# Kernel tuning notes

Hardware: AMD Instinct MI355X
Metric: run time of the kernel (lower is better)

The kernel has to match this reference:

```python
import jax, jax.numpy as jnp
import numpy as np

NTA = 65536   # total atoms across all crystals
NC = 1024     # number of crystals
NO = 256      # descriptor output dim (desc.NO)
H = 332       # int(NO * 1.3) hidden dim of per-species MLP
S = 4         # number of species


def setup_inputs() -> dict:
    key = jax.random.key(0)
    ks = jax.random.split(key, 8)
    symbols = jax.random.randint(ks[0], (NTA,), 0, S)
    positions = jax.random.normal(ks[1], (NTA, 3), jnp.float32) * 3.0
    cells = jax.random.normal(ks[2], (NC, 3, 3), jnp.float32)
    pbcs = jnp.ones((NC, 3), dtype=bool)
    energyidx = jnp.arange(NC)
    crystalidx = jax.random.randint(ks[3], (NTA,), 0, NC)
    # stand-in descriptor projection (replaces external REANN desc module)
    Wd = jax.random.normal(ks[4], (3, NO), jnp.float32) * 0.5
    # stacked per-species MLP params: Linear(NO,H) -> SiLU -> Linear(H,1)
    W1 = jax.random.normal(ks[5], (S, NO, H), jnp.float32) / np.sqrt(NO).astype(np.float32)
    b1 = jnp.zeros((S, H), jnp.float32)
    W2 = jax.random.normal(ks[6], (S, H), jnp.float32) / np.sqrt(H).astype(np.float32)
    b2 = jnp.zeros((S,), jnp.float32)
    return {
        "symbols": symbols, "positions": positions, "cells": cells,
        "pbcs": pbcs, "energyidx": energyidx, "crystalidx": crystalidx,
        "Wd": Wd, "W1": W1, "b1": b1, "W2": W2, "b2": b2,
    }


def _atomic_energies(positions, symbols, Wd, W1, b1, W2, b2):
    # stand-in descriptor: [NTA, NO]
    feat = jnp.tanh(positions @ Wd)
    n_species = W1.shape[0]
    e = jnp.zeros((positions.shape[0],), feat.dtype)
    # species-routed small MLPs: dense compute + select (fixed small loop over species)
    for s in range(n_species):
        h = jax.nn.silu(feat @ W1[s] + b1[s])       # [NTA, H]
        es = h @ W2[s] + b2[s]                      # [NTA]
        e = jnp.where(symbols == s, es, e)
    return e


def reference(symbols, positions, cells, pbcs, energyidx, crystalidx, Wd, W1, b1, W2, b2):
    num_crystals = energyidx.shape[0]

    def total_energy(pos):
        en = _atomic_energies(pos, symbols, Wd, W1, b1, W2, b2)   # [NTA]
        E = jax.ops.segment_sum(en, crystalidx, num_segments=num_crystals)  # [NC]
        return jnp.sum(E), (en, E)

    # torch code: forces = grad(sum(energy), positions)  (positive gradient)
    forces, (energies, energy) = jax.grad(total_energy, has_aux=True)(positions)
    return (energies, energy, forces)
```

## Files before the change

kernel.cpp:

```cpp
#include <hip/hip_runtime.h>

#define NTA 65536
#define NC 1024
#define NO 256
#define HDIM 332
#define HP 352
#define NSP 4
#define NOUT (NTA + NC + NTA*3)
#define SORT_CAP (NTA + 4*128)

#define DP_STRIDE 720
#define LDS_MAIN  159744

typedef __attribute__((ext_vector_type(8))) short short8;
typedef __attribute__((ext_vector_type(4))) float f32x4;

#define OFF_CNT   0
#define OFF_CUR   64
#define OFF_START 128
#define OFF_FLAG  160
#define OFF_SORT  256
#define OFF_B1P   264448
#define OFF_W2P   270080
#define OFF_W1T   275712
#define OFF_W1P   996608
#define OFF_FACC  1717504

__device__ __forceinline__ unsigned short f2bf(float f){
  unsigned int u = __builtin_bit_cast(unsigned int, f);
  u += 0x7fffu + ((u>>16)&1u);
  return (unsigned short)(u>>16);
}
__device__ __forceinline__ float bf2f(unsigned short h){
  unsigned int u = ((unsigned int)h)<<16;
  return __builtin_bit_cast(float, u);
}
__device__ __forceinline__ float ldf(const void* p, int idx, int isbf){
  if (isbf) return bf2f(((const unsigned short*)p)[idx]);
  return ((const float*)p)[idx];
}
__device__ __forceinline__ float rcpf(float x){ return __builtin_amdgcn_rcpf(x); }

__global__ void k_init(float* __restrict__ acc, unsigned int* __restrict__ wshead,
                       int* __restrict__ sorted, const unsigned short* __restrict__ posu,
                       unsigned int* __restrict__ flag){
  int i = blockIdx.x*256 + threadIdx.x;
  acc[i] = 0.f;
  if (i < 32) wshead[i] = 0u;
  if (i < SORT_CAP) sorted[i] = -1;
  if (blockIdx.x == 1027 && threadIdx.x < 64){
    unsigned short u = posu[2*threadIdx.x];
    int e = (u>>7)&0xFF;
    bool inr = (e >= 110 && e <= 140);
    unsigned long long m = __ballot(inr);
    if (threadIdx.x == 0) flag[0] = (__popcll(m) >= 32) ? 1u : 0u;
  }
}

__global__ void k_count(const int* __restrict__ sym, unsigned int* __restrict__ cnt){
  __shared__ unsigned int h[NSP];
  int t = threadIdx.x;
  if (t < NSP) h[t] = 0u;
  __syncthreads();
  int i = blockIdx.x*256 + t;
  atomicAdd(&h[sym[i]], 1u);
  __syncthreads();
  if (t < NSP) atomicAdd(&cnt[t], h[t]);
}

__global__ void k_starts(const unsigned int* __restrict__ cnt, int* __restrict__ starts){
  if (threadIdx.x == 0){
    int a = 0; starts[0] = 0;
    for (int s=0;s<NSP;s++){ a += (int)(((cnt[s]+127u)>>7)<<7); starts[s+1] = a; }
  }
}

__global__ void k_scatter(const int* __restrict__ sym, const int* __restrict__ starts,
                          unsigned int* __restrict__ cur, int* __restrict__ sorted){
  int i = blockIdx.x*256 + threadIdx.x;
  int s = sym[i];
  int lane = threadIdx.x & 63;
  #pragma unroll
  for (int ss=0; ss<NSP; ss++){
    unsigned long long m = __ballot(s==ss);
    if (s == ss){
      int leader = __builtin_ctzll(m);
      int cw = __popcll(m);
      unsigned int b = 0;
      if (lane == leader) b = atomicAdd(&cur[ss], (unsigned int)cw);
      b = (unsigned int)__shfl((int)b, leader);
      int rank = __popcll(m & ((1ull<<lane) - 1ull));
      sorted[starts[ss] + (int)b + rank] = i;
    }
  }
}

__global__ void k_prepw(const void* __restrict__ W1, const void* __restrict__ b1,
                        const void* __restrict__ W2, const unsigned int* __restrict__ flag,
                        unsigned short* __restrict__ w1t, unsigned short* __restrict__ w1p,
                        float* __restrict__ b1p, float* __restrict__ w2p){
  const int isbf = (int)flag[0];
  int idx = blockIdx.x*256 + threadIdx.x;
  int s = idx / (HP*NO);
  int r = idx % (HP*NO);
  int j = r / NO;
  int i = r % NO;
  float v = (j < HDIM) ? ldf(W1, (s*NO + i)*HDIM + j, isbf) : 0.f;
  unsigned short hv = f2bf(v);
  w1t[(s*HP + j)*NO + i] = hv;
  w1p[(s*NO + i)*HP + j] = hv;
  if (i == 0){
    b1p[s*HP + j] = (j < HDIM) ? ldf(b1, s*HDIM + j, isbf) : 0.f;
    w2p[s*HP + j] = (j < HDIM) ? ldf(W2, s*HDIM + j, isbf) : 0.f;
  }
}

__global__ __launch_bounds__(512,2) void k_main(
    const int* __restrict__ sorted, const int* __restrict__ starts,
    const void* __restrict__ pos, const void* __restrict__ Wd,
    const unsigned short* __restrict__ W1T, const unsigned short* __restrict__ W1P,
    const float* __restrict__ b1p, const float* __restrict__ w2p,
    const void* __restrict__ b2g, const int* __restrict__ crys,
    const unsigned int* __restrict__ flag,
    float* __restrict__ Eatom, float* __restrict__ Ecry, float* __restrict__ forces)
{
  extern __shared__ char smem[];
  ushort4* wdT = (ushort4*)smem;
  char* featB  = smem + 2048;
  char* dpB    = smem + 2048 + 65536;
  float* Epart = (float*)dpB;
  float* Fpart = (float*)(dpB + 4096);

  const int base = blockIdx.x*128;
  if (base >= starts[4]) return;
  const int isbf = (int)flag[0];
  int sp = 0;
  #pragma unroll
  for (int s=1;s<NSP;s++) sp = (base >= starts[s]) ? s : sp;

  const int tid = threadIdx.x;
  const int l = tid & 63;
  const int w = tid >> 6;
  const int c = l & 15;
  const int g = l >> 4;

  if (tid < 256){
    float x = ldf(Wd, tid, isbf), y = ldf(Wd, NO+tid, isbf), z = ldf(Wd, 2*NO+tid, isbf);
    ushort4 u; u.x = f2bf(x); u.y = f2bf(y); u.z = f2bf(z); u.w = 0;
    wdT[tid] = u;
  }
  __syncthreads();

  {
    const int m = tid & 127;
    const int h = tid >> 7;
    int a = sorted[base + m];
    float px=0.f, py=0.f, pz=0.f;
    if (a >= 0){ px = ldf(pos,3*a,isbf); py = ldf(pos,3*a+1,isbf); pz = ldf(pos,3*a+2,isbf); }
    const int swz = (m&7)<<4;
    char* rowp = featB + m*512;
    #pragma unroll
    for (int k8=0;k8<8;k8++){
      int i0 = h*64 + k8*8;
      unsigned int pk[4];
      #pragma unroll
      for (int p2=0;p2<4;p2++){
        unsigned short hv[2];
        #pragma unroll
        for (int e2=0;e2<2;e2++){
          ushort4 wv = wdT[i0 + 2*p2 + e2];
          float v = px*bf2f(wv.x) + py*bf2f(wv.y) + pz*bf2f(wv.z);
          float e = __expf(2.f*v);
          hv[e2] = f2bf(1.f - 2.f*rcpf(e+1.f));
        }
        pk[p2] = (unsigned int)hv[0] | ((unsigned int)hv[1]<<16);
      }
      *(uint4*)(rowp + ((i0*2) ^ swz)) = make_uint4(pk[0],pk[1],pk[2],pk[3]);
    }
  }
  __syncthreads();

  const unsigned short* W1Ts = W1T + sp*HP*NO;
  const int fr0 = (w<6) ? w*3 : 18 + (w-6)*2;
  const int nT  = (w<6) ? 3 : 2;
  f32x4 acc[3][8];
  #pragma unroll
  for (int t=0;t<3;t++)
    #pragma unroll
    for (int nb=0;nb<8;nb++) acc[t][nb] = f32x4{0.f,0.f,0.f,0.f};

  #pragma unroll
  for (int kk=0; kk<8; kk++){
    short8 bfr[8];
    #pragma unroll
    for (int nb=0;nb<8;nb++){
      int m = nb*16 + c;
      bfr[nb] = *(const short8*)(featB + m*512 + ((kk*64 + g*16) ^ ((m&7)<<4)));
    }
    #pragma unroll
    for (int t=0;t<3;t++){
      if (t < nT){
        const short8 afr = *(const short8*)((const char*)W1Ts + ((fr0+t)*16 + c)*512 + kk*64 + g*16);
        #pragma unroll
        for (int nb=0;nb<8;nb++)
          acc[t][nb] = __builtin_amdgcn_mfma_f32_16x16x32_bf16(afr, bfr[nb], acc[t][nb], 0,0,0);
      }
    }
  }

  const float* b1s = b1p + sp*HP;
  const float* w2s = w2p + sp*HP;
  float esp[8] = {0.f,0.f,0.f,0.f,0.f,0.f,0.f,0.f};
  #pragma unroll
  for (int t=0;t<3;t++){
    if (t < nT){
      const int j0 = (fr0+t)*16 + g*4;
      const float4 b1v = *(const float4*)(b1s + j0);
      const float4 w2v = *(const float4*)(w2s + j0);
      const float* b1a = (const float*)&b1v;
      const float* w2a = (const float*)&w2v;
      #pragma unroll
      for (int nb=0;nb<8;nb++){
        const int m = nb*16 + c;
        unsigned short dph[4];
        #pragma unroll
        for (int q=0;q<4;q++){
          float pre = acc[t][nb][q] + b1a[q];
          float sg = rcpf(1.f + __expf(-pre));
          float h = pre*sg;
          esp[nb] += h*w2a[q];
          float dsl = sg*(1.f + pre*(1.f - sg));
          dph[q] = f2bf(w2a[q]*dsl);
        }
        *(uint2*)(dpB + m*DP_STRIDE + j0*2) =
            make_uint2((unsigned)dph[0] | ((unsigned)dph[1]<<16),
                       (unsigned)dph[2] | ((unsigned)dph[3]<<16));
      }
    }
  }
  float e8[8];
  #pragma unroll
  for (int nb=0;nb<8;nb++){
    float e = esp[nb];
    e += __shfl_xor(e, 16);
    e += __shfl_xor(e, 32);
    e8[nb] = e;
  }
  __syncthreads();

  const unsigned short* W1Ps = W1P + sp*NO*HP;
  f32x4 acc2[2][8];
  #pragma unroll
  for (int t2=0;t2<2;t2++)
    #pragma unroll
    for (int nb=0;nb<8;nb++) acc2[t2][nb] = f32x4{0.f,0.f,0.f,0.f};

  #pragma unroll
  for (int kk=0; kk<11; kk++){
    short8 bfr[8];
    #pragma unroll
    for (int nb=0;nb<8;nb++){
      int m = nb*16 + c;
      bfr[nb] = *(const short8*)(dpB + m*DP_STRIDE + kk*64 + g*16);
    }
    #pragma unroll
    for (int t2=0;t2<2;t2++){
      const short8 afr = *(const short8*)((const char*)W1Ps + ((2*w+t2)*16 + c)*704 + kk*64 + g*16);
      #pragma unroll
      for (int nb=0;nb<8;nb++)
        acc2[t2][nb] = __builtin_amdgcn_mfma_f32_16x16x32_bf16(afr, bfr[nb], acc2[t2][nb], 0,0,0);
    }
  }

  float fax[8], fay[8], faz[8];
  #pragma unroll
  for (int nb=0;nb<8;nb++){ fax[nb]=0.f; fay[nb]=0.f; faz[nb]=0.f; }
  #pragma unroll
  for (int t2=0;t2<2;t2++){
    const int i0 = (2*w+t2)*16 + g*4;
    #pragma unroll
    for (int nb=0;nb<8;nb++){
      const int m = nb*16 + c;
      uint2 fpk = *(const uint2*)(featB + m*512 + ((i0*2) ^ ((m&7)<<4)));
      unsigned short fh[4];
      fh[0] = (unsigned short)(fpk.x & 0xffffu); fh[1] = (unsigned short)(fpk.x >> 16);
      fh[2] = (unsigned short)(fpk.y & 0xffffu); fh[3] = (unsigned short)(fpk.y >> 16);
      #pragma unroll
      for (int q=0;q<4;q++){
        float ff = bf2f(fh[q]);
        float gsc = acc2[t2][nb][q] * (1.f - ff*ff);
        ushort4 wv = wdT[i0 + q];
        fax[nb] += gsc*bf2f(wv.x);
        fay[nb] += gsc*bf2f(wv.y);
        faz[nb] += gsc*bf2f(wv.z);
      }
    }
  }
  #pragma unroll
  for (int nb=0;nb<8;nb++){
    float x = fax[nb], y = fay[nb], z = faz[nb];
    x += __shfl_xor(x, 16); x += __shfl_xor(x, 32);
    y += __shfl_xor(y, 16); y += __shfl_xor(y, 32);
    z += __shfl_xor(z, 16); z += __shfl_xor(z, 32);
    fax[nb] = x; fay[nb] = y; faz[nb] = z;
  }
  __syncthreads();

  if (g == 0){
    #pragma unroll
    for (int nb=0;nb<8;nb++){
      const int m = nb*16 + c;
      Epart[w*128 + m] = e8[nb];
      Fpart[(w*128 + m)*3 + 0] = fax[nb];
      Fpart[(w*128 + m)*3 + 1] = fay[nb];
      Fpart[(w*128 + m)*3 + 2] = faz[nb];
    }
  }
  __syncthreads();

  if (tid < 128){
    int a = sorted[base + tid];
    if (a >= 0){
      float E = ldf(b2g, sp, isbf);
      float fx = 0.f, fy = 0.f, fz = 0.f;
      #pragma unroll
      for (int ww=0; ww<8; ww++){
        E  += Epart[ww*128 + tid];
        fx += Fpart[(ww*128 + tid)*3 + 0];
        fy += Fpart[(ww*128 + tid)*3 + 1];
        fz += Fpart[(ww*128 + tid)*3 + 2];
      }
      Eatom[a] = E;
      atomicAdd(&Ecry[crys[a]], E);
      forces[3*a+0] = fx;
      forces[3*a+1] = fy;
      forces[3*a+2] = fz;
    }
  }
}

__global__ void k_out(const float* __restrict__ Eatom, const float* __restrict__ Ecry,
                      const float* __restrict__ Facc, float* __restrict__ out){
  int i = blockIdx.x*256 + threadIdx.x;
  float v;
  if (i < NTA)            v = Eatom[i];
  else if (i < NTA + NC)  v = Ecry[i - NTA];
  else                    v = Facc[i - NTA - NC];
  out[i] = v;
}

extern "C" void kernel_launch(void* const* d_in, const int* in_sizes, int n_in,
                              void* d_out, int out_size, void* d_ws, size_t ws_size,
                              hipStream_t stream) {
  const int*   symbols    = (const int*)  d_in[0];
  const void*  positions  = d_in[1];
  const int*   crystalidx = (const int*)  d_in[5];
  const void*  Wd         = d_in[6];
  const void*  W1         = d_in[7];
  const void*  b1         = d_in[8];
  const void*  W2         = d_in[9];
  const void*  b2         = d_in[10];
  float* dout = (float*)d_out;

  char* ws = (char*)d_ws;
  unsigned int* cnt    = (unsigned int*)(ws + OFF_CNT);
  unsigned int* cur    = (unsigned int*)(ws + OFF_CUR);
  int*          starts = (int*)         (ws + OFF_START);
  unsigned int* flag   = (unsigned int*)(ws + OFF_FLAG);
  int*          sorted = (int*)         (ws + OFF_SORT);
  float*        b1p    = (float*)       (ws + OFF_B1P);
  float*        w2p    = (float*)       (ws + OFF_W2P);
  unsigned short* w1t  = (unsigned short*)(ws + OFF_W1T);
  unsigned short* w1pp = (unsigned short*)(ws + OFF_W1P);
  float*        Facc   = (float*)       (ws + OFF_FACC);
  float*        Eatom  = Facc + NTA*3;
  float*        Ecry   = Eatom + NTA;

  hipFuncSetAttribute((const void*)k_main,
                      hipFuncAttributeMaxDynamicSharedMemorySize, LDS_MAIN);

  k_init   <<<1028,256, 0, stream>>>(Facc, (unsigned int*)ws, sorted,
                                     (const unsigned short*)positions, flag);
  k_count  <<<256, 256, 0, stream>>>(symbols, cnt);
  k_starts <<<1,    64, 0, stream>>>(cnt, starts);
  k_scatter<<<256, 256, 0, stream>>>(symbols, starts, cur, sorted);
  k_prepw  <<<1408,256, 0, stream>>>(W1, b1, W2, flag, w1t, w1pp, b1p, w2p);
  k_main   <<<516, 512, LDS_MAIN, stream>>>(sorted, starts, positions, Wd,
                                            w1t, w1pp, b1p, w2p, b2, crystalidx,
                                            flag, Eatom, Ecry, Facc);
  k_out    <<<1028,256, 0, stream>>>(Eatom, Ecry, Facc, dout);
}
```

Baseline: 153.0 us.

## Fuse setup kernels, write outputs directly, tile weight transpose, prefetch A fragments

New measurement: 139.1 us. 9.1% less time.

```diff
diff --git a/kernel.cpp b/kernel.cpp
--- a/kernel.cpp
+++ b/kernel.cpp
@@ -24,7 +24,6 @@
 #define OFF_W2P   270080
 #define OFF_W1T   275712
 #define OFF_W1P   996608
-#define OFF_FACC  1717504
 
 __device__ __forceinline__ unsigned short f2bf(float f){
   unsigned int u = __builtin_bit_cast(unsigned int, f);
@@ -41,45 +40,46 @@
 }
 __device__ __forceinline__ float rcpf(float x){ return __builtin_amdgcn_rcpf(x); }
 
-__global__ void k_init(float* __restrict__ acc, unsigned int* __restrict__ wshead,
-                       int* __restrict__ sorted, const unsigned short* __restrict__ posu,
-                       unsigned int* __restrict__ flag){
-  int i = blockIdx.x*256 + threadIdx.x;
-  acc[i] = 0.f;
-  if (i < 32) wshead[i] = 0u;
+__global__ void k_init2(const int* __restrict__ sym, unsigned int* __restrict__ cnt,
+                        int* __restrict__ sorted, const unsigned short* __restrict__ posu,
+                        unsigned int* __restrict__ flag, float* __restrict__ dout){
+  __shared__ unsigned int h[NSP];
+  int t = threadIdx.x;
+  if (t < NSP) h[t] = 0u;
+  __syncthreads();
+  int i = blockIdx.x*256 + t;
   if (i < SORT_CAP) sorted[i] = -1;
-  if (blockIdx.x == 1027 && threadIdx.x < 64){
-    unsigned short u = posu[2*threadIdx.x];
+  if (i < NC) dout[NTA + i] = 0.f;
+  if (i < NTA) atomicAdd(&h[sym[i]], 1u);
+  __syncthreads();
+  if (t < NSP && h[t]) atomicAdd(&cnt[t], h[t]);
+  if (blockIdx.x == 257 && t < 64){
+    unsigned short u = posu[2*t];
     int e = (u>>7)&0xFF;
     bool inr = (e >= 110 && e <= 140);
     unsigned long long m = __ballot(inr);
-    if (threadIdx.x == 0) flag[0] = (__popcll(m) >= 32) ? 1u : 0u;
-  }
-}
-
-__global__ void k_count(const int* __restrict__ sym, unsigned int* __restrict__ cnt){
-  __shared__ unsigned int h[NSP];
+    if (t == 0) flag[0] = (__popcll(m) >= 32) ? 1u : 0u;
+  }
+}
+
+__global__ void k_scatter2(const int* __restrict__ sym, const unsigned int* __restrict__ cnt,
+                           unsigned int* __restrict__ cur, int* __restrict__ sorted,
+                           int* __restrict__ gstarts){
+  __shared__ int sl[NSP+1];
   int t = threadIdx.x;
-  if (t < NSP) h[t] = 0u;
+  if (t == 0){
+    int a = 0; sl[0] = 0;
+    #pragma unroll
+    for (int s=0;s<NSP;s++){ a += (int)(((cnt[s]+127u)>>7)<<7); sl[s+1] = a; }
+    if (blockIdx.x == 0){
+      #pragma unroll
+      for (int s=0;s<=NSP;s++) gstarts[s] = sl[s];
+    }
+  }
   __syncthreads();
   int i = blockIdx.x*256 + t;
-  atomicAdd(&h[sym[i]], 1u);
-  __syncthreads();
-  if (t < NSP) atomicAdd(&cnt[t], h[t]);
-}
-
-__global__ void k_starts(const unsigned int* __restrict__ cnt, int* __restrict__ starts){
-  if (threadIdx.x == 0){
-    int a = 0; starts[0] = 0;
-    for (int s=0;s<NSP;s++){ a += (int)(((cnt[s]+127u)>>7)<<7); starts[s+1] = a; }
-  }
-}
-
-__global__ void k_scatter(const int* __restrict__ sym, const int* __restrict__ starts,
-                          unsigned int* __restrict__ cur, int* __restrict__ sorted){
-  int i = blockIdx.x*256 + threadIdx.x;
   int s = sym[i];
-  int lane = threadIdx.x & 63;
+  int lane = t & 63;
   #pragma unroll
   for (int ss=0; ss<NSP; ss++){
     unsigned long long m = __ballot(s==ss);
@@ -90,26 +90,46 @@
       if (lane == leader) b = atomicAdd(&cur[ss], (unsigned int)cw);
       b = (unsigned int)__shfl((int)b, leader);
       int rank = __popcll(m & ((1ull<<lane) - 1ull));
-      sorted[starts[ss] + (int)b + rank] = i;
-    }
-  }
-}
-
-__global__ void k_prepw(const void* __restrict__ W1, const void* __restrict__ b1,
-                        const void* __restrict__ W2, const unsigned int* __restrict__ flag,
-                        unsigned short* __restrict__ w1t, unsigned short* __restrict__ w1p,
-                        float* __restrict__ b1p, float* __restrict__ w2p){
+      sorted[sl[ss] + (int)b + rank] = i;
+    }
+  }
+}
+
+__global__ void k_prepw2(const void* __restrict__ W1, const void* __restrict__ b1,
+                         const void* __restrict__ W2, const unsigned int* __restrict__ flag,
+                         unsigned short* __restrict__ w1t, unsigned short* __restrict__ w1p,
+                         float* __restrict__ b1p, float* __restrict__ w2p){
+  __shared__ unsigned short T[32][36];
   const int isbf = (int)flag[0];
-  int idx = blockIdx.x*256 + threadIdx.x;
-  int s = idx / (HP*NO);
-  int r = idx % (HP*NO);
-  int j = r / NO;
-  int i = r % NO;
-  float v = (j < HDIM) ? ldf(W1, (s*NO + i)*HDIM + j, isbf) : 0.f;
-  unsigned short hv = f2bf(v);
-  w1t[(s*HP + j)*NO + i] = hv;
-  w1p[(s*NO + i)*HP + j] = hv;
-  if (i == 0){
+  const int bid = blockIdx.x;
+  const int s  = bid / 88;
+  const int jt = (bid % 88) / 8;
+  const int it = bid % 8;
+  const int t = threadIdx.x;
+  {
+    const int il = t >> 3;
+    const int j4 = (t & 7) * 4;
+    const int i = it*32 + il;
+    #pragma unroll
+    for (int e=0;e<4;e++){
+      int j = jt*32 + j4 + e;
+      float v = (j < HDIM) ? ldf(W1, (s*NO + i)*HDIM + j, isbf) : 0.f;
+      T[il][j4+e] = f2bf(v);
+    }
+  }
+  __syncthreads();
+  {
+    const int jl = t >> 3;
+    const int i4 = (t & 7) * 4;
+    ushort4 v; v.x = T[i4][jl]; v.y = T[i4+1][jl]; v.z = T[i4+2][jl]; v.w = T[i4+3][jl];
+    *(ushort4*)&w1t[(s*HP + jt*32 + jl)*NO + it*32 + i4] = v;
+    const int il = t >> 3;
+    const int j4 = (t & 7) * 4;
+    ushort4 u; u.x = T[il][j4]; u.y = T[il][j4+1]; u.z = T[il][j4+2]; u.w = T[il][j4+3];
+    *(ushort4*)&w1p[(s*NO + it*32 + il)*HP + jt*32 + j4] = u;
+  }
+  if (it == 0 && t < 32){
+    int j = jt*32 + t;
     b1p[s*HP + j] = (j < HDIM) ? ldf(b1, s*HDIM + j, isbf) : 0.f;
     w2p[s*HP + j] = (j < HDIM) ? ldf(W2, s*HDIM + j, isbf) : 0.f;
   }
@@ -121,8 +141,7 @@
     const unsigned short* __restrict__ W1T, const unsigned short* __restrict__ W1P,
     const float* __restrict__ b1p, const float* __restrict__ w2p,
     const void* __restrict__ b2g, const int* __restrict__ crys,
-    const unsigned int* __restrict__ flag,
-    float* __restrict__ Eatom, float* __restrict__ Ecry, float* __restrict__ forces)
+    const unsigned int* __restrict__ flag, float* __restrict__ dout)
 {
   extern __shared__ char smem[];
   ushort4* wdT = (ushort4*)smem;
@@ -189,8 +208,21 @@
     #pragma unroll
     for (int nb=0;nb<8;nb++) acc[t][nb] = f32x4{0.f,0.f,0.f,0.f};
 
+  short8 pf[3];
+  #pragma unroll
+  for (int t=0;t<3;t++)
+    if (t < nT) pf[t] = *(const short8*)((const char*)W1Ts + ((fr0+t)*16 + c)*512 + g*16);
+
   #pragma unroll
   for (int kk=0; kk<8; kk++){
+    short8 cur[3];
+    #pragma unroll
+    for (int t=0;t<3;t++) cur[t] = pf[t];
+    if (kk < 7){
+      #pragma unroll
+      for (int t=0;t<3;t++)
+        if (t < nT) pf[t] = *(const short8*)((const char*)W1Ts + ((fr0+t)*16 + c)*512 + (kk+1)*64 + g*16);
+    }
     short8 bfr[8];
     #pragma unroll
     for (int nb=0;nb<8;nb++){
@@ -200,10 +232,9 @@
     #pragma unroll
     for (int t=0;t<3;t++){
       if (t < nT){
-        const short8 afr = *(const short8*)((const char*)W1Ts + ((fr0+t)*16 + c)*512 + kk*64 + g*16);
         #pragma unroll
         for (int nb=0;nb<8;nb++)
-          acc[t][nb] = __builtin_amdgcn_mfma_f32_16x16x32_bf16(afr, bfr[nb], acc[t][nb], 0,0,0);
+          acc[t][nb] = __builtin_amdgcn_mfma_f32_16x16x32_bf16(cur[t], bfr[nb], acc[t][nb], 0,0,0);
       }
     }
   }
@@ -255,8 +286,21 @@
     #pragma unroll
     for (int nb=0;nb<8;nb++) acc2[t2][nb] = f32x4{0.f,0.f,0.f,0.f};
 
+  short8 pf2[2];
+  #pragma unroll
+  for (int t2=0;t2<2;t2++)
+    pf2[t2] = *(const short8*)((const char*)W1Ps + ((2*w+t2)*16 + c)*704 + g*16);
+
   #pragma unroll
   for (int kk=0; kk<11; kk++){
+    short8 cur2[2];
+    #pragma unroll
+    for (int t2=0;t2<2;t2++) cur2[t2] = pf2[t2];
+    if (kk < 10){
+      #pragma unroll
+      for (int t2=0;t2<2;t2++)
+        pf2[t2] = *(const short8*)((const char*)W1Ps + ((2*w+t2)*16 + c)*704 + (kk+1)*64 + g*16);
+    }
     short8 bfr[8];
     #pragma unroll
     for (int nb=0;nb<8;nb++){
@@ -265,10 +309,9 @@
     }
     #pragma unroll
     for (int t2=0;t2<2;t2++){
-      const short8 afr = *(const short8*)((const char*)W1Ps + ((2*w+t2)*16 + c)*704 + kk*64 + g*16);
       #pragma unroll
       for (int nb=0;nb<8;nb++)
-        acc2[t2][nb] = __builtin_amdgcn_mfma_f32_16x16x32_bf16(afr, bfr[nb], acc2[t2][nb], 0,0,0);
+        acc2[t2][nb] = __builtin_amdgcn_mfma_f32_16x16x32_bf16(cur2[t2], bfr[nb], acc2[t2][nb], 0,0,0);
     }
   }
 
@@ -330,23 +373,13 @@
         fy += Fpart[(ww*128 + tid)*3 + 1];
         fz += Fpart[(ww*128 + tid)*3 + 2];
       }
-      Eatom[a] = E;
-      atomicAdd(&Ecry[crys[a]], E);
-      forces[3*a+0] = fx;
-      forces[3*a+1] = fy;
-      forces[3*a+2] = fz;
-    }
-  }
-}
-
-__global__ void k_out(const float* __restrict__ Eatom, const float* __restrict__ Ecry,
-                      const float* __restrict__ Facc, float* __restrict__ out){
-  int i = blockIdx.x*256 + threadIdx.x;
-  float v;
-  if (i < NTA)            v = Eatom[i];
-  else if (i < NTA + NC)  v = Ecry[i - NTA];
-  else                    v = Facc[i - NTA - NC];
-  out[i] = v;
+      dout[a] = E;
+      atomicAdd(&dout[NTA + crys[a]], E);
+      dout[NTA + NC + 3*a + 0] = fx;
+      dout[NTA + NC + 3*a + 1] = fy;
+      dout[NTA + NC + 3*a + 2] = fz;
+    }
+  }
 }
 
 extern "C" void kernel_launch(void* const* d_in, const int* in_sizes, int n_in,
@@ -372,21 +405,16 @@
   float*        w2p    = (float*)       (ws + OFF_W2P);
   unsigned short* w1t  = (unsigned short*)(ws + OFF_W1T);
   unsigned short* w1pp = (unsigned short*)(ws + OFF_W1P);
-  float*        Facc   = (float*)       (ws + OFF_FACC);
-  float*        Eatom  = Facc + NTA*3;
-  float*        Ecry   = Eatom + NTA;
 
   hipFuncSetAttribute((const void*)k_main,
                       hipFuncAttributeMaxDynamicSharedMemorySize, LDS_MAIN);
 
-  k_init   <<<1028,256, 0, stream>>>(Facc, (unsigned int*)ws, sorted,
-                                     (const unsigned short*)positions, flag);
-  k_count  <<<256, 256, 0, stream>>>(symbols, cnt);
-  k_starts <<<1,    64, 0, stream>>>(cnt, starts);
-  k_scatter<<<256, 256, 0, stream>>>(symbols, starts, cur, sorted);
-  k_prepw  <<<1408,256, 0, stream>>>(W1, b1, W2, flag, w1t, w1pp, b1p, w2p);
-  k_main   <<<516, 512, LDS_MAIN, stream>>>(sorted, starts, positions, Wd,
-                                            w1t, w1pp, b1p, w2p, b2, crystalidx,
-                                            flag, Eatom, Ecry, Facc);
-  k_out    <<<1028,256, 0, stream>>>(Eatom, Ecry, Facc, dout);
-}
+  hipMemsetAsync(ws, 0, 256, stream);
+  k_init2   <<<258, 256, 0, stream>>>(symbols, cnt, sorted,
+                                      (const unsigned short*)positions, flag, dout);
+  k_scatter2<<<256, 256, 0, stream>>>(symbols, cnt, cur, sorted, starts);
+  k_prepw2  <<<352, 256, 0, stream>>>(W1, b1, W2, flag, w1t, w1pp, b1p, w2p);
+  k_main    <<<516, 512, LDS_MAIN, stream>>>(sorted, starts, positions, Wd,
+                                             w1t, w1pp, b1p, w2p, b2, crystalidx,
+                                             flag, dout);
+}
```
